# Performance work log

Measured on AMD Instinct MI355X. Metric: run time of the kernel, lower is better.

The kernel has to match this reference:

```python
import jax, jax.numpy as jnp
import numpy as np

N_NODES = 50000
IN_DIM = 128
HIDDEN = 64
N_EDGES = 1600000


def setup_inputs() -> dict:
    key = jax.random.key(0)
    k1, k2, k3, k4, k5, k6 = jax.random.split(key, 6)
    x_proj = jax.random.normal(k1, (N_NODES, IN_DIM), dtype=jnp.float32)
    edge_index = jax.random.randint(k2, (2, N_EDGES), 0, N_NODES, dtype=jnp.int64)
    # Linear(2*in_dim, hidden): PyTorch stores weight as [out, in]; keep that layout.
    lim1 = 1.0 / np.sqrt(2 * IN_DIM)
    w1 = jax.random.uniform(k3, (HIDDEN, 2 * IN_DIM), minval=-lim1, maxval=lim1, dtype=jnp.float32)
    b1 = jax.random.uniform(k4, (HIDDEN,), minval=-lim1, maxval=lim1, dtype=jnp.float32)
    lim2 = 1.0 / np.sqrt(HIDDEN)
    w2 = jax.random.uniform(k5, (1, HIDDEN), minval=-lim2, maxval=lim2, dtype=jnp.float32)
    b2 = jax.random.uniform(k6, (1,), minval=-lim2, maxval=lim2, dtype=jnp.float32)
    return {"x_proj": x_proj, "edge_index": edge_index, "w1": w1, "b1": b1, "w2": w2, "b2": b2}


def reference(x_proj, edge_index, w1, b1, w2, b2):
    # Chunking in the original is only for memory; math == single vectorized pass.
    row, col = edge_index[0], edge_index[1]
    h = jnp.concatenate([x_proj[row], x_proj[col]], axis=1)  # [E, 2*in_dim]
    h = jax.nn.relu(h @ w1.T + b1)                            # [E, hidden]
    s = jax.nn.sigmoid(h @ w2.T + b2).squeeze(-1)             # [E]
    return s
```

## Files before the change

### kernel.cpp

```cpp
#include <hip/hip_runtime.h>
#include <hip/hip_bf16.h>


typedef __attribute__((ext_vector_type(8))) short bf16x8;
typedef __attribute__((ext_vector_type(4))) float f32x4;
typedef __attribute__((ext_vector_type(4))) unsigned short u16x4;

#define IN_DIM 128
#define HIDDEN 64

__device__ __forceinline__ short f2bf(float f) {
    union { float f; unsigned u; } v; v.f = f;
    unsigned r = v.u + 0x7FFFu + ((v.u >> 16) & 1u);
    return (short)(r >> 16);
}

__device__ __forceinline__ bf16x8 pack8(const float4& lo, const float4& hi) {
    bf16x8 b;
    b[0] = f2bf(lo.x); b[1] = f2bf(lo.y); b[2] = f2bf(lo.z); b[3] = f2bf(lo.w);
    b[4] = f2bf(hi.x); b[5] = f2bf(hi.y); b[6] = f2bf(hi.z); b[7] = f2bf(hi.w);
    return b;
}

__global__ __launch_bounds__(256) void node_proj_kernel(
    const float* __restrict__ x,
    const float* __restrict__ w1,
    const float* __restrict__ b1,
    unsigned short* __restrict__ ytab,
    int N, int ntiles)
{
    __shared__ short wfrag[2048 * 8];

    {
        int v = threadIdx.x;
#pragma unroll
        for (int j = 0; j < 8; ++j) {
            int f = v * 64 + j * 8;
            int r = f >> 8;
            int k = f & 255;
            float4 lo = *(const float4*)(w1 + f);
            float4 hi = *(const float4*)(w1 + f + 4);
            int o, kk, g;
            if (k < IN_DIM) { o = r;          kk = k >> 5;             g = (k & 31) >> 3; }
            else            { o = r + HIDDEN; kk = (k - IN_DIM) >> 5;  g = ((k - IN_DIM) & 31) >> 3; }
            int dt = o >> 4, m = o & 15;
            int lane = g * 16 + m;
            *(bf16x8*)&wfrag[((dt * 4 + kk) * 64 + lane) * 8] = pack8(lo, hi);
        }
    }
    __syncthreads();

    int wave = (int)((blockIdx.x * blockDim.x + threadIdx.x) >> 6);
    if (wave >= ntiles) return;

    int lane = threadIdx.x & 63;
    int m = lane & 15;
    int g = lane >> 4;
    int n0 = wave * 16;

    int node = n0 + m;
    bool valid = node < N;
    int nclamp = valid ? node : N - 1;
    const float* xr = x + (size_t)nclamp * IN_DIM;

    bf16x8 xf[4];
#pragma unroll
    for (int kk = 0; kk < 4; ++kk) {
        int k0 = kk * 32 + g * 8;
        float4 lo = *(const float4*)(xr + k0);
        float4 hi = *(const float4*)(xr + k0 + 4);
        xf[kk] = pack8(lo, hi);
    }

    f32x4 acc[8] = {};
#pragma unroll
    for (int dt = 0; dt < 8; ++dt) {
#pragma unroll
        for (int kk = 0; kk < 4; ++kk) {
            bf16x8 wf = *(const bf16x8*)&wfrag[((dt * 4 + kk) * 64 + lane) * 8];
            acc[dt] = __builtin_amdgcn_mfma_f32_16x16x32_bf16(wf, xf[kk], acc[dt], 0, 0, 0);
        }
    }

    if (valid) {
        unsigned short* yrow = ytab + (size_t)node * IN_DIM;
#pragma unroll
        for (int dt = 0; dt < 8; ++dt) {
            float4 b4;
            if (dt < 4) b4 = *(const float4*)(b1 + dt * 16 + g * 4);
            else        b4 = make_float4(0.f, 0.f, 0.f, 0.f);
            u16x4 s;
            s[0] = (unsigned short)f2bf(acc[dt][0] + b4.x);
            s[1] = (unsigned short)f2bf(acc[dt][1] + b4.y);
            s[2] = (unsigned short)f2bf(acc[dt][2] + b4.z);
            s[3] = (unsigned short)f2bf(acc[dt][3] + b4.w);
            *(u16x4*)(yrow + dt * 16 + g * 4) = s;
        }
    }
}

__device__ __forceinline__ float dimpair(unsigned u1, unsigned u2, float wlo, float whi, float acc) {
    float a0 = __uint_as_float(u1 << 16);
    float a1 = __uint_as_float(u1 & 0xffff0000u);
    float b0 = __uint_as_float(u2 << 16);
    float b1v = __uint_as_float(u2 & 0xffff0000u);
    float h0 = fmaxf(a0 + b0, 0.f);
    float h1 = fmaxf(a1 + b1v, 0.f);
    acc = fmaf(h0, wlo, acc);
    acc = fmaf(h1, whi, acc);
    return acc;
}

__device__ __forceinline__ float edge_dot(const uint4& ua, const uint4& ub,
                                          const float4& w2a, const float4& w2b) {
    float acc = 0.f;
    acc = dimpair(ua.x, ub.x, w2a.x, w2a.y, acc);
    acc = dimpair(ua.y, ub.y, w2a.z, w2a.w, acc);
    acc = dimpair(ua.z, ub.z, w2b.x, w2b.y, acc);
    acc = dimpair(ua.w, ub.w, w2b.z, w2b.w, acc);
    acc += __shfl_xor(acc, 1);
    acc += __shfl_xor(acc, 2);
    acc += __shfl_xor(acc, 4);
    return acc;
}

__device__ __forceinline__ float sigmoidf(float z) {
    return 1.f / (1.f + __expf(-z));
}

__global__ __launch_bounds__(256) void edge_kernel(
    const int* __restrict__ ei,
    const unsigned short* __restrict__ ytab,
    const float* __restrict__ w2,
    const float* __restrict__ b2,
    float* __restrict__ out,
    int E)
{
    int t = (int)(blockIdx.x * 256 + threadIdx.x);
    int q = t >> 3;
    int sub = t & 7;
    int e0 = q * 4;
    if (e0 >= E) return;

    const char* yb = (const char*)ytab;
    float4 w2a = *((const float4*)w2 + sub * 2);
    float4 w2b = *((const float4*)w2 + sub * 2 + 1);
    int so = sub << 4;

    if (e0 + 4 <= E) {
        int4 rows = *(const int4*)(ei + e0);
        int4 cols = *(const int4*)(ei + E + e0);
        uint4 a0 = *(const uint4*)(yb + ((rows.x << 8) + so));
        uint4 a1 = *(const uint4*)(yb + ((rows.y << 8) + so));
        uint4 a2 = *(const uint4*)(yb + ((rows.z << 8) + so));
        uint4 a3 = *(const uint4*)(yb + ((rows.w << 8) + so));
        uint4 c0 = *(const uint4*)(yb + ((cols.x << 8) + 128 + so));
        uint4 c1 = *(const uint4*)(yb + ((cols.y << 8) + 128 + so));
        uint4 c2 = *(const uint4*)(yb + ((cols.z << 8) + 128 + so));
        uint4 c3 = *(const uint4*)(yb + ((cols.w << 8) + 128 + so));

        float z0 = edge_dot(a0, c0, w2a, w2b);
        float z1 = edge_dot(a1, c1, w2a, w2b);
        float z2 = edge_dot(a2, c2, w2a, w2b);
        float z3 = edge_dot(a3, c3, w2a, w2b);

        if (sub == 0) {
            float bb = b2[0];
            float4 s;
            s.x = sigmoidf(z0 + bb);
            s.y = sigmoidf(z1 + bb);
            s.z = sigmoidf(z2 + bb);
            s.w = sigmoidf(z3 + bb);
            *(float4*)(out + e0) = s;
        }
    } else {
        float bb = b2[0];
        for (int e = e0; e < E; ++e) {
            int row = ei[e];
            int col = ei[E + e];
            uint4 ua = *(const uint4*)(yb + ((row << 8) + so));
            uint4 ub = *(const uint4*)(yb + ((col << 8) + 128 + so));
            float z = edge_dot(ua, ub, w2a, w2b);
            if (sub == 0) out[e] = sigmoidf(z + bb);
        }
    }
}

extern "C" void kernel_launch(void* const* d_in, const int* in_sizes, int n_in,
                              void* d_out, int out_size, void* d_ws, size_t ws_size,
                              hipStream_t stream) {
    const float* x  = (const float*)d_in[0];
    const int*   ei = (const int*)d_in[1];
    const float* w1 = (const float*)d_in[2];
    const float* b1 = (const float*)d_in[3];
    const float* w2 = (const float*)d_in[4];
    const float* b2 = (const float*)d_in[5];
    float* out = (float*)d_out;

    int N = in_sizes[0] / IN_DIM;
    int E = in_sizes[1] / 2;

    unsigned short* ytab = (unsigned short*)d_ws;

    int ntiles = (N + 15) / 16;
    int nblocks = (ntiles + 3) / 4;
    node_proj_kernel<<<nblocks, 256, 0, stream>>>(x, w1, b1, ytab, N, ntiles);

    long long quads = ((long long)E + 3) / 4;
    long long tthreads = quads * 8;
    int eblocks = (int)((tthreads + 255) / 256);
    edge_kernel<<<eblocks, 256, 0, stream>>>(ei, ytab, w2, b2, out, E);
}
```

Before: 65.35 us.

## Precompute bf16 weight fragments, persist node-proj grid, process 8 edges per thread group

Moves the w1 fp32-to-bf16 fragment conversion into a separate one-block kernel, so each node-projection block only copies a prepacked table into LDS. The node-projection kernel becomes a grid-stride loop over 512 blocks, so that LDS staging is paid once per block rather than once per 4 tiles. The edge kernel handles 8 edges per 8-lane group instead of 4, putting more independent gathers in flight. This adds an extra kernel launch, increases register pressure in the edge kernel, and halves the edge grid size.

```diff
diff --git a/kernel.cpp b/kernel.cpp
--- a/kernel.cpp
+++ b/kernel.cpp
@@ -9,22 +9,44 @@
 #define IN_DIM 128
 #define HIDDEN 64
 
-__device__ __forceinline__ short f2bf(float f) {
-    union { float f; unsigned u; } v; v.f = f;
-    unsigned r = v.u + 0x7FFFu + ((v.u >> 16) & 1u);
-    return (short)(r >> 16);
+__device__ __forceinline__ unsigned short bfbits(float f) {
+    __hip_bfloat16 h = __float2bfloat16(f);
+    return __builtin_bit_cast(unsigned short, h);
 }
 
 __device__ __forceinline__ bf16x8 pack8(const float4& lo, const float4& hi) {
     bf16x8 b;
-    b[0] = f2bf(lo.x); b[1] = f2bf(lo.y); b[2] = f2bf(lo.z); b[3] = f2bf(lo.w);
-    b[4] = f2bf(hi.x); b[5] = f2bf(hi.y); b[6] = f2bf(hi.z); b[7] = f2bf(hi.w);
+    b[0] = (short)bfbits(lo.x); b[1] = (short)bfbits(lo.y);
+    b[2] = (short)bfbits(lo.z); b[3] = (short)bfbits(lo.w);
+    b[4] = (short)bfbits(hi.x); b[5] = (short)bfbits(hi.y);
+    b[6] = (short)bfbits(hi.z); b[7] = (short)bfbits(hi.w);
     return b;
+}
+
+__global__ __launch_bounds__(256) void convert_w1_kernel(
+    const float* __restrict__ w1,
+    unsigned short* __restrict__ wtab)
+{
+    int v = threadIdx.x;
+#pragma unroll
+    for (int j = 0; j < 8; ++j) {
+        int f = v * 64 + j * 8;
+        int r = f >> 8;
+        int k = f & 255;
+        float4 lo = *(const float4*)(w1 + f);
+        float4 hi = *(const float4*)(w1 + f + 4);
+        int o, kk, g;
+        if (k < IN_DIM) { o = r;          kk = k >> 5;             g = (k & 31) >> 3; }
+        else            { o = r + HIDDEN; kk = (k - IN_DIM) >> 5;  g = ((k - IN_DIM) & 31) >> 3; }
+        int dt = o >> 4, m = o & 15;
+        int lane = g * 16 + m;
+        *(bf16x8*)&wtab[((dt * 4 + kk) * 64 + lane) * 8] = pack8(lo, hi);
+    }
 }
 
 __global__ __launch_bounds__(256) void node_proj_kernel(
     const float* __restrict__ x,
-    const float* __restrict__ w1,
+    const unsigned short* __restrict__ wtab,
     const float* __restrict__ b1,
     unsigned short* __restrict__ ytab,
     int N, int ntiles)
@@ -32,69 +54,60 @@
     __shared__ short wfrag[2048 * 8];
 
     {
+        uint4* dst = (uint4*)wfrag;
+        const uint4* src = (const uint4*)wtab;
         int v = threadIdx.x;
 #pragma unroll
-        for (int j = 0; j < 8; ++j) {
-            int f = v * 64 + j * 8;
-            int r = f >> 8;
-            int k = f & 255;
-            float4 lo = *(const float4*)(w1 + f);
-            float4 hi = *(const float4*)(w1 + f + 4);
-            int o, kk, g;
-            if (k < IN_DIM) { o = r;          kk = k >> 5;             g = (k & 31) >> 3; }
-            else            { o = r + HIDDEN; kk = (k - IN_DIM) >> 5;  g = ((k - IN_DIM) & 31) >> 3; }
-            int dt = o >> 4, m = o & 15;
-            int lane = g * 16 + m;
-            *(bf16x8*)&wfrag[((dt * 4 + kk) * 64 + lane) * 8] = pack8(lo, hi);
-        }
+        for (int j = 0; j < 8; ++j) dst[v + j * 256] = src[v + j * 256];
     }
     __syncthreads();
-
-    int wave = (int)((blockIdx.x * blockDim.x + threadIdx.x) >> 6);
-    if (wave >= ntiles) return;
 
     int lane = threadIdx.x & 63;
     int m = lane & 15;
     int g = lane >> 4;
-    int n0 = wave * 16;
-
-    int node = n0 + m;
-    bool valid = node < N;
-    int nclamp = valid ? node : N - 1;
-    const float* xr = x + (size_t)nclamp * IN_DIM;
-
-    bf16x8 xf[4];
-#pragma unroll
-    for (int kk = 0; kk < 4; ++kk) {
-        int k0 = kk * 32 + g * 8;
-        float4 lo = *(const float4*)(xr + k0);
-        float4 hi = *(const float4*)(xr + k0 + 4);
-        xf[kk] = pack8(lo, hi);
-    }
-
-    f32x4 acc[8] = {};
-#pragma unroll
-    for (int dt = 0; dt < 8; ++dt) {
+    int gwave = (int)blockIdx.x * 4 + (threadIdx.x >> 6);
+    int wstride = (int)gridDim.x * 4;
+
+    for (int t = gwave; t < ntiles; t += wstride) {
+        int n0 = t * 16;
+        int node = n0 + m;
+        bool valid = node < N;
+        int nc = valid ? node : N - 1;
+        const float* xr = x + (size_t)nc * IN_DIM;
+
+        bf16x8 xf[4];
 #pragma unroll
         for (int kk = 0; kk < 4; ++kk) {
-            bf16x8 wf = *(const bf16x8*)&wfrag[((dt * 4 + kk) * 64 + lane) * 8];
-            acc[dt] = __builtin_amdgcn_mfma_f32_16x16x32_bf16(wf, xf[kk], acc[dt], 0, 0, 0);
-        }
-    }
-
-    if (valid) {
-        unsigned short* yrow = ytab + (size_t)node * IN_DIM;
+            int k0 = kk * 32 + g * 8;
+            float4 lo = *(const float4*)(xr + k0);
+            float4 hi = *(const float4*)(xr + k0 + 4);
+            xf[kk] = pack8(lo, hi);
+        }
+
+        f32x4 acc[8] = {};
 #pragma unroll
         for (int dt = 0; dt < 8; ++dt) {
-            float4 b4;
-            if (dt < 4) b4 = *(const float4*)(b1 + dt * 16 + g * 4);
-            else        b4 = make_float4(0.f, 0.f, 0.f, 0.f);
-            u16x4 s;
-            s[0] = (unsigned short)f2bf(acc[dt][0] + b4.x);
-            s[1] = (unsigned short)f2bf(acc[dt][1] + b4.y);
-            s[2] = (unsigned short)f2bf(acc[dt][2] + b4.z);
-            s[3] = (unsigned short)f2bf(acc[dt][3] + b4.w);
-            *(u16x4*)(yrow + dt * 16 + g * 4) = s;
+#pragma unroll
+            for (int kk = 0; kk < 4; ++kk) {
+                bf16x8 wf = *(const bf16x8*)&wfrag[((dt * 4 + kk) * 64 + lane) * 8];
+                acc[dt] = __builtin_amdgcn_mfma_f32_16x16x32_bf16(wf, xf[kk], acc[dt], 0, 0, 0);
+            }
+        }
+
+        if (valid) {
+            unsigned short* yrow = ytab + (size_t)node * IN_DIM;
+#pragma unroll
+            for (int dt = 0; dt < 8; ++dt) {
+                float4 b4;
+                if (dt < 4) b4 = *(const float4*)(b1 + dt * 16 + g * 4);
+                else        b4 = make_float4(0.f, 0.f, 0.f, 0.f);
+                u16x4 s;
+                s[0] = bfbits(acc[dt][0] + b4.x);
+                s[1] = bfbits(acc[dt][1] + b4.y);
+                s[2] = bfbits(acc[dt][2] + b4.z);
+                s[3] = bfbits(acc[dt][3] + b4.w);
+                *(u16x4*)(yrow + dt * 16 + g * 4) = s;
+            }
         }
     }
 }
@@ -139,7 +152,7 @@
     int t = (int)(blockIdx.x * 256 + threadIdx.x);
     int q = t >> 3;
     int sub = t & 7;
-    int e0 = q * 4;
+    int e0 = q * 8;
     if (e0 >= E) return;
 
     const char* yb = (const char*)ytab;
@@ -147,31 +160,50 @@
     float4 w2b = *((const float4*)w2 + sub * 2 + 1);
     int so = sub << 4;
 
-    if (e0 + 4 <= E) {
-        int4 rows = *(const int4*)(ei + e0);
-        int4 cols = *(const int4*)(ei + E + e0);
-        uint4 a0 = *(const uint4*)(yb + ((rows.x << 8) + so));
-        uint4 a1 = *(const uint4*)(yb + ((rows.y << 8) + so));
-        uint4 a2 = *(const uint4*)(yb + ((rows.z << 8) + so));
-        uint4 a3 = *(const uint4*)(yb + ((rows.w << 8) + so));
-        uint4 c0 = *(const uint4*)(yb + ((cols.x << 8) + 128 + so));
-        uint4 c1 = *(const uint4*)(yb + ((cols.y << 8) + 128 + so));
-        uint4 c2 = *(const uint4*)(yb + ((cols.z << 8) + 128 + so));
-        uint4 c3 = *(const uint4*)(yb + ((cols.w << 8) + 128 + so));
+    if (e0 + 8 <= E) {
+        int4 ra = *(const int4*)(ei + e0);
+        int4 rb = *(const int4*)(ei + e0 + 4);
+        int4 ca = *(const int4*)(ei + E + e0);
+        int4 cb = *(const int4*)(ei + E + e0 + 4);
+        uint4 a0 = *(const uint4*)(yb + ((ra.x << 8) + so));
+        uint4 a1 = *(const uint4*)(yb + ((ra.y << 8) + so));
+        uint4 a2 = *(const uint4*)(yb + ((ra.z << 8) + so));
+        uint4 a3 = *(const uint4*)(yb + ((ra.w << 8) + so));
+        uint4 a4 = *(const uint4*)(yb + ((rb.x << 8) + so));
+        uint4 a5 = *(const uint4*)(yb + ((rb.y << 8) + so));
+        uint4 a6 = *(const uint4*)(yb + ((rb.z << 8) + so));
+        uint4 a7 = *(const uint4*)(yb + ((rb.w << 8) + so));
+        uint4 c0 = *(const uint4*)(yb + ((ca.x << 8) + 128 + so));
+        uint4 c1 = *(const uint4*)(yb + ((ca.y << 8) + 128 + so));
+        uint4 c2 = *(const uint4*)(yb + ((ca.z << 8) + 128 + so));
+        uint4 c3 = *(const uint4*)(yb + ((ca.w << 8) + 128 + so));
+        uint4 c4 = *(const uint4*)(yb + ((cb.x << 8) + 128 + so));
+        uint4 c5 = *(const uint4*)(yb + ((cb.y << 8) + 128 + so));
+        uint4 c6 = *(const uint4*)(yb + ((cb.z << 8) + 128 + so));
+        uint4 c7 = *(const uint4*)(yb + ((cb.w << 8) + 128 + so));
 
         float z0 = edge_dot(a0, c0, w2a, w2b);
         float z1 = edge_dot(a1, c1, w2a, w2b);
         float z2 = edge_dot(a2, c2, w2a, w2b);
         float z3 = edge_dot(a3, c3, w2a, w2b);
+        float z4 = edge_dot(a4, c4, w2a, w2b);
+        float z5 = edge_dot(a5, c5, w2a, w2b);
+        float z6 = edge_dot(a6, c6, w2a, w2b);
+        float z7 = edge_dot(a7, c7, w2a, w2b);
 
         if (sub == 0) {
             float bb = b2[0];
-            float4 s;
-            s.x = sigmoidf(z0 + bb);
-            s.y = sigmoidf(z1 + bb);
-            s.z = sigmoidf(z2 + bb);
-            s.w = sigmoidf(z3 + bb);
-            *(float4*)(out + e0) = s;
+            float4 s0, s1;
+            s0.x = sigmoidf(z0 + bb);
+            s0.y = sigmoidf(z1 + bb);
+            s0.z = sigmoidf(z2 + bb);
+            s0.w = sigmoidf(z3 + bb);
+            s1.x = sigmoidf(z4 + bb);
+            s1.y = sigmoidf(z5 + bb);
+            s1.z = sigmoidf(z6 + bb);
+            s1.w = sigmoidf(z7 + bb);
+            *(float4*)(out + e0) = s0;
+            *(float4*)(out + e0 + 4) = s1;
         }
     } else {
         float bb = b2[0];
@@ -200,14 +232,16 @@
     int N = in_sizes[0] / IN_DIM;
     int E = in_sizes[1] / 2;
 
-    unsigned short* ytab = (unsigned short*)d_ws;
+    unsigned short* wtab = (unsigned short*)d_ws;
+    unsigned short* ytab = (unsigned short*)d_ws + 16384;
+
+    convert_w1_kernel<<<1, 256, 0, stream>>>(w1, wtab);
 
     int ntiles = (N + 15) / 16;
-    int nblocks = (ntiles + 3) / 4;
-    node_proj_kernel<<<nblocks, 256, 0, stream>>>(x, w1, b1, ytab, N, ntiles);
-
-    long long quads = ((long long)E + 3) / 4;
-    long long tthreads = quads * 8;
+    node_proj_kernel<<<512, 256, 0, stream>>>(x, wtab, b1, ytab, N, ntiles);
+
+    long long octs = ((long long)E + 7) / 8;
+    long long tthreads = octs * 8;
     int eblocks = (int)((tthreads + 255) / 256);
     edge_kernel<<<eblocks, 256, 0, stream>>>(ei, ytab, w2, b2, out, E);
 }
```

Result: no change. 65.03 us (-0.5%).
